# Performance work log

Measured on AMD Instinct MI355X. Metric: run time of the kernel, lower is better.

Reference implementation:

```python
import jax, jax.numpy as jnp
import numpy as np

B, S, H, E = 64, 1024, 256, 256

def setup_inputs() -> dict:
    key = jax.random.key(0)
    k = jax.random.split(key, 6)
    scale = 1.0 / np.sqrt(H)
    return {
        "data_alpha": jax.random.normal(k[0], (B, S, H), jnp.float32),
        "data_beta": jax.random.normal(k[1], (B, S, H), jnp.float32),
        "data_embed": jax.random.normal(k[2], (B, S, E), jnp.float32),
        "data_mask": jnp.ones((B, S), jnp.float32),
        "Wb": jax.random.normal(k[3], (E, H), jnp.float32) * scale,
        "bb": jnp.zeros((E,), jnp.float32),
        "Wa": jax.random.normal(k[4], (H,), jnp.float32) * scale,
        "ba": jnp.zeros((1,), jnp.float32),
    }

def reference(data_alpha, data_beta, data_embed, data_mask, Wb, bb, Wa, ba):
    # beta gates: tanh(Linear(H->E))  [B,S,E]
    beta_w = jnp.tanh(jnp.einsum('bsh,eh->bse', data_beta, Wb) + bb)
    # alpha logits: Linear(H->1)  [B,S]
    corr = jnp.einsum('bsh,h->bs', data_alpha, Wa) + ba
    attn = jnp.exp(corr)[:, None, :]                       # [B,1,S]
    seq = data_alpha.shape[1]
    flag = jnp.triu(jnp.ones((seq, seq), data_alpha.dtype))[None]  # j >= i
    ef = flag * data_mask[:, None, :]                      # [B,S,S]
    num = attn * ef                                        # [B,S,S]
    acc = jnp.sum(num, axis=-1, keepdims=True) + 1e-10     # [B,S,1]
    alpha = num / acc                                      # [B,S,S]
    ew = beta_w * data_embed                               # [B,S,E]
    return jnp.einsum('bij,bje->bie', alpha, ew)           # [B,S,E]
```

## Files before the change

### kernel.cpp

```cpp
#include <hip/hip_runtime.h>
#include <hip/hip_bf16.h>

#define S_LEN 1024
#define B_DIM 64
#define H_DIM 256
#define E_DIM 256
#define M_ROWS (B_DIM * S_LEN)

#define CT_COLS 64
#define NCT (E_DIM / CT_COLS)
#define CHUNK_R 256
#define NCHUNKS (S_LEN / CHUNK_R)
#define NTHREADS 1024
#define NWAVES 16

#define BPAD 264

typedef __attribute__((ext_vector_type(8))) short bf16x8;
typedef __attribute__((ext_vector_type(4))) float f32x4;

__device__ __forceinline__ short cvt1(float f) {
  union { float ff; unsigned u; } t;
  t.ff = f;
  unsigned u = t.u;
  return (short)((u + 0x7fffu + ((u >> 16) & 1u)) >> 16);
}

__device__ __forceinline__ bf16x8 cvt8v(float4 x, float4 y) {
  bf16x8 r;
  r[0] = cvt1(x.x); r[1] = cvt1(x.y); r[2] = cvt1(x.z); r[3] = cvt1(x.w);
  r[4] = cvt1(y.x); r[5] = cvt1(y.y); r[6] = cvt1(y.z); r[7] = cvt1(y.w);
  return r;
}

__device__ __forceinline__ float fast_tanh(float x) {
  float t = __expf(2.0f * x);
  return 1.0f - 2.0f * __builtin_amdgcn_rcpf(t + 1.0f);
}

__global__ __launch_bounds__(256) void w_kernel(
    const float* __restrict__ alpha, const float* __restrict__ Wa,
    const float* __restrict__ ba, const float* __restrict__ mask,
    float* __restrict__ wv) {
  int wave = threadIdx.x >> 6, lane = threadIdx.x & 63;
  long long row = (long long)blockIdx.x * 4 + wave;
  const float4 a = reinterpret_cast<const float4*>(alpha + row * H_DIM)[lane];
  const float4 wa = reinterpret_cast<const float4*>(Wa)[lane];
  float d = a.x * wa.x + a.y * wa.y + a.z * wa.z + a.w * wa.w;
#pragma unroll
  for (int m = 32; m; m >>= 1) d += __shfl_xor(d, m);
  if (lane == 0) wv[row] = expf(d + ba[0]) * mask[row];
}

__global__ __launch_bounds__(1024) void acc_kernel(
    const float* __restrict__ wv, float* __restrict__ invacc) {
  __shared__ float s[2][S_LEN];
  int b = blockIdx.x, i = threadIdx.x;
  s[0][i] = wv[b * S_LEN + i];
  __syncthreads();
  int src = 0;
#pragma unroll
  for (int off = 1; off < S_LEN; off <<= 1) {
    float v = s[src][i];
    if (i + off < S_LEN) v += s[src][i + off];
    s[src ^ 1][i] = v;
    __syncthreads();
    src ^= 1;
  }
  invacc[b * S_LEN + i] = 1.0f / (s[src][i] + 1e-10f);
}

__global__ __launch_bounds__(NTHREADS, 8) void fused_kernel(
    const float* __restrict__ beta, const float* __restrict__ Wb,
    const float* __restrict__ bb, const float* __restrict__ embed,
    const float* __restrict__ wv, const float* __restrict__ invacc,
    float* __restrict__ out) {
  __shared__ short Bsm[CT_COLS * BPAD];
  __shared__ float segsum[NWAVES * CT_COLS];
  __shared__ float carry[CT_COLS];

  const int tid = threadIdx.x;
  const int hw = blockIdx.x;
  const int b = (hw & 7) + (((hw >> 3) & 7) << 3);
  const int colbase = (hw >> 6) * CT_COLS;

  {
    int c = tid >> 4, ks = (tid & 15) * 16;
    const float4* src =
        reinterpret_cast<const float4*>(Wb + (long long)(colbase + c) * H_DIM + ks);
    float4 v0 = src[0], v1 = src[1], v2 = src[2], v3 = src[3];
    *reinterpret_cast<bf16x8*>(&Bsm[c * BPAD + ks]) = cvt8v(v0, v1);
    *reinterpret_cast<bf16x8*>(&Bsm[c * BPAD + ks + 8]) = cvt8v(v2, v3);
  }
  if (tid < CT_COLS) carry[tid] = 0.f;
  __syncthreads();

  const int wave = tid >> 6, lane = tid & 63;
  const int rl = lane & 15, kg = lane >> 4;

  for (int chunk = NCHUNKS - 1; chunk >= 0; --chunk) {
    const long long rowstart = (long long)b * S_LEN + chunk * CHUNK_R;
    const long long r0 = rowstart + wave * 16;
    const float* aptr = beta + (r0 + rl) * H_DIM + kg * 8;

    f32x4 acc[4] = {{0.f,0.f,0.f,0.f},{0.f,0.f,0.f,0.f},
                    {0.f,0.f,0.f,0.f},{0.f,0.f,0.f,0.f}};

    float4 a0[2], a1[2];
    a0[0] = *reinterpret_cast<const float4*>(aptr + 0);
    a1[0] = *reinterpret_cast<const float4*>(aptr + 4);
    a0[1] = *reinterpret_cast<const float4*>(aptr + 32);
    a1[1] = *reinterpret_cast<const float4*>(aptr + 36);
#pragma unroll
    for (int ks = 0; ks < 8; ++ks) {
      float4 na0 = {0.f,0.f,0.f,0.f}, na1 = {0.f,0.f,0.f,0.f};
      if (ks < 6) {
        na0 = *reinterpret_cast<const float4*>(aptr + (ks + 2) * 32);
        na1 = *reinterpret_cast<const float4*>(aptr + (ks + 2) * 32 + 4);
      }
      bf16x8 am = cvt8v(a0[0], a1[0]);
      int kb = ks * 32 + kg * 8;
#pragma unroll
      for (int j = 0; j < 4; ++j) {
        bf16x8 bn = *reinterpret_cast<const bf16x8*>(&Bsm[(j * 16 + rl) * BPAD + kb]);
        acc[j] = __builtin_amdgcn_mfma_f32_16x16x32_bf16(am, bn, acc[j], 0, 0, 0);
      }
      a0[0] = a0[1]; a1[0] = a1[1];
      a0[1] = na0;   a1[1] = na1;
    }

    float wvq[4], inv[4];
#pragma unroll
    for (int q = 0; q < 4; ++q) {
      long long r = r0 + kg * 4 + q;
      wvq[q] = wv[r];
      inv[q] = invacc[r];
    }

    float sv[4][4];
    float off[4];
    float cn[4];
#pragma unroll
    for (int j = 0; j < 4; ++j) {
      int c = j * 16 + rl;
      int e = colbase + c;
      float bbe = bb[e];
      float p[4];
#pragma unroll
      for (int q = 0; q < 4; ++q) {
        long long r = r0 + kg * 4 + q;
        p[q] = wvq[q] * fast_tanh(acc[j][q] + bbe) * embed[r * E_DIM + e];
      }
      sv[j][3] = p[3];
      sv[j][2] = p[2] + sv[j][3];
      sv[j][1] = p[1] + sv[j][2];
      sv[j][0] = p[0] + sv[j][1];
      float gtot = sv[j][0];
      float t16 = __shfl_xor(gtot, 16);
      float t32 = __shfl_xor(gtot, 32);
      float t48 = __shfl_xor(gtot, 48);
      off[j] = (kg == 0) ? (t16 + t32 + t48)
             : (kg == 1) ? (t32 + t48)
             : (kg == 2) ? t16 : 0.f;
      float wtot = gtot + t16 + t32 + t48;
      if (kg == 0) segsum[wave * CT_COLS + c] = wtot;
    }
    __syncthreads();

#pragma unroll
    for (int j = 0; j < 4; ++j) {
      int c = j * 16 + rl;
      float segoff = carry[c];
      for (int w2 = wave + 1; w2 < NWAVES; ++w2)
        segoff += segsum[w2 * CT_COLS + c];
      off[j] += segoff;
      cn[j] = off[j] + sv[j][0];
#pragma unroll
      for (int q = 0; q < 4; ++q) {
        long long r = r0 + kg * 4 + q;
        out[r * E_DIM + colbase + c] = (sv[j][q] + off[j]) * inv[q];
      }
    }
    __syncthreads();
    if (wave == 0 && kg == 0) {
#pragma unroll
      for (int j = 0; j < 4; ++j) carry[j * 16 + rl] = cn[j];
    }
  }
}

extern "C" void kernel_launch(void* const* d_in, const int* in_sizes, int n_in,
                              void* d_out, int out_size, void* d_ws,
                              size_t ws_size, hipStream_t stream) {
  const float* alpha = (const float*)d_in[0];
  const float* beta = (const float*)d_in[1];
  const float* embed = (const float*)d_in[2];
  const float* mask = (const float*)d_in[3];
  const float* Wb = (const float*)d_in[4];
  const float* bb = (const float*)d_in[5];
  const float* Wa = (const float*)d_in[6];
  const float* ba = (const float*)d_in[7];
  float* out = (float*)d_out;

  float* wv = (float*)d_ws;
  float* invacc = wv + M_ROWS;

  w_kernel<<<M_ROWS / 4, 256, 0, stream>>>(alpha, Wa, ba, mask, wv);
  acc_kernel<<<B_DIM, 1024, 0, stream>>>(wv, invacc);
  fused_kernel<<<B_DIM * NCT, NTHREADS, 0, stream>>>(beta, Wb, bb, embed, wv,
                                                     invacc, out);
}
```

Baseline: 259.5 us.

## Prefetch next chunk's beta, embed and weights; double-buffer scan scratch to drop a barrier

Loads of the next chunk's beta rows, embed values, wv and invacc are issued during the current chunk's compute, so global-memory latency overlaps the MFMA and scan work. The segment-sum and carry arrays are double-buffered by chunk parity, which removes the second __syncthreads per chunk. The bias loads are hoisted out of the loop, the cross-wave offset loop is fully unrolled with a predicate, and the occupancy hint in launch bounds drops from 8 to 4. The extra prefetch registers raise register pressure, and the lower occupancy hint changes how many waves the compiler plans for.

Result: faster. 242.9 us (-6.4%).

```diff
diff --git a/kernel.cpp b/kernel.cpp
--- a/kernel.cpp
+++ b/kernel.cpp
@@ -70,14 +70,14 @@
   invacc[b * S_LEN + i] = 1.0f / (s[src][i] + 1e-10f);
 }
 
-__global__ __launch_bounds__(NTHREADS, 8) void fused_kernel(
+__global__ __launch_bounds__(NTHREADS, 4) void fused_kernel(
     const float* __restrict__ beta, const float* __restrict__ Wb,
     const float* __restrict__ bb, const float* __restrict__ embed,
     const float* __restrict__ wv, const float* __restrict__ invacc,
     float* __restrict__ out) {
   __shared__ short Bsm[CT_COLS * BPAD];
-  __shared__ float segsum[NWAVES * CT_COLS];
-  __shared__ float carry[CT_COLS];
+  __shared__ float segsum[2][NWAVES * CT_COLS];
+  __shared__ float carry[2][CT_COLS];
 
   const int tid = threadIdx.x;
   const int hw = blockIdx.x;
@@ -92,65 +92,89 @@
     *reinterpret_cast<bf16x8*>(&Bsm[c * BPAD + ks]) = cvt8v(v0, v1);
     *reinterpret_cast<bf16x8*>(&Bsm[c * BPAD + ks + 8]) = cvt8v(v2, v3);
   }
-  if (tid < CT_COLS) carry[tid] = 0.f;
+  if (tid < CT_COLS) { carry[0][tid] = 0.f; carry[1][tid] = 0.f; }
   __syncthreads();
 
   const int wave = tid >> 6, lane = tid & 63;
   const int rl = lane & 15, kg = lane >> 4;
 
+  float bbv[4];
+#pragma unroll
+  for (int j = 0; j < 4; ++j) bbv[j] = bb[colbase + j * 16 + rl];
+
+  const float* ap =
+      beta + ((long long)b * S_LEN + 3 * CHUNK_R + wave * 16 + rl) * H_DIM + kg * 8;
+  float4 pa0 = *reinterpret_cast<const float4*>(ap + 0);
+  float4 pa1 = *reinterpret_cast<const float4*>(ap + 4);
+  float4 pb0 = *reinterpret_cast<const float4*>(ap + 32);
+  float4 pb1 = *reinterpret_cast<const float4*>(ap + 36);
+
+  float emb[4][4], wvq[4], inv[4];
+  {
+    const long long r0 = (long long)b * S_LEN + 3 * CHUNK_R + wave * 16 + kg * 4;
+#pragma unroll
+    for (int q = 0; q < 4; ++q) {
+      wvq[q] = wv[r0 + q];
+      inv[q] = invacc[r0 + q];
+#pragma unroll
+      for (int j = 0; j < 4; ++j)
+        emb[q][j] = embed[(r0 + q) * E_DIM + colbase + j * 16 + rl];
+    }
+  }
+
   for (int chunk = NCHUNKS - 1; chunk >= 0; --chunk) {
+    const int nc = (chunk > 0) ? chunk - 1 : 0;
     const long long rowstart = (long long)b * S_LEN + chunk * CHUNK_R;
     const long long r0 = rowstart + wave * 16;
-    const float* aptr = beta + (r0 + rl) * H_DIM + kg * 8;
+    const float* ap_next =
+        beta + ((long long)b * S_LEN + nc * CHUNK_R + wave * 16 + rl) * H_DIM + kg * 8;
 
     f32x4 acc[4] = {{0.f,0.f,0.f,0.f},{0.f,0.f,0.f,0.f},
                     {0.f,0.f,0.f,0.f},{0.f,0.f,0.f,0.f}};
 
-    float4 a0[2], a1[2];
-    a0[0] = *reinterpret_cast<const float4*>(aptr + 0);
-    a1[0] = *reinterpret_cast<const float4*>(aptr + 4);
-    a0[1] = *reinterpret_cast<const float4*>(aptr + 32);
-    a1[1] = *reinterpret_cast<const float4*>(aptr + 36);
 #pragma unroll
     for (int ks = 0; ks < 8; ++ks) {
-      float4 na0 = {0.f,0.f,0.f,0.f}, na1 = {0.f,0.f,0.f,0.f};
+      float4 n0, n1;
       if (ks < 6) {
-        na0 = *reinterpret_cast<const float4*>(aptr + (ks + 2) * 32);
-        na1 = *reinterpret_cast<const float4*>(aptr + (ks + 2) * 32 + 4);
-      }
-      bf16x8 am = cvt8v(a0[0], a1[0]);
+        n0 = *reinterpret_cast<const float4*>(ap + (ks + 2) * 32);
+        n1 = *reinterpret_cast<const float4*>(ap + (ks + 2) * 32 + 4);
+      } else {
+        n0 = *reinterpret_cast<const float4*>(ap_next + (ks - 6) * 32);
+        n1 = *reinterpret_cast<const float4*>(ap_next + (ks - 6) * 32 + 4);
+      }
+      bf16x8 am = cvt8v(pa0, pa1);
       int kb = ks * 32 + kg * 8;
 #pragma unroll
       for (int j = 0; j < 4; ++j) {
         bf16x8 bn = *reinterpret_cast<const bf16x8*>(&Bsm[(j * 16 + rl) * BPAD + kb]);
         acc[j] = __builtin_amdgcn_mfma_f32_16x16x32_bf16(am, bn, acc[j], 0, 0, 0);
       }
-      a0[0] = a0[1]; a1[0] = a1[1];
-      a0[1] = na0;   a1[1] = na1;
-    }
-
-    float wvq[4], inv[4];
-#pragma unroll
-    for (int q = 0; q < 4; ++q) {
-      long long r = r0 + kg * 4 + q;
-      wvq[q] = wv[r];
-      inv[q] = invacc[r];
-    }
-
-    float sv[4][4];
-    float off[4];
-    float cn[4];
+      pa0 = pb0; pa1 = pb1; pb0 = n0; pb1 = n1;
+    }
+    ap = ap_next;
+
+    float emb_n[4][4], wvq_n[4], inv_n[4];
+    {
+      const long long rn = (long long)b * S_LEN + nc * CHUNK_R + wave * 16 + kg * 4;
+#pragma unroll
+      for (int q = 0; q < 4; ++q) {
+        wvq_n[q] = wv[rn + q];
+        inv_n[q] = invacc[rn + q];
+#pragma unroll
+        for (int j = 0; j < 4; ++j)
+          emb_n[q][j] = embed[(rn + q) * E_DIM + colbase + j * 16 + rl];
+      }
+    }
+
+    const int rd = chunk & 1;
+    float sv[4][4], off[4];
 #pragma unroll
     for (int j = 0; j < 4; ++j) {
       int c = j * 16 + rl;
-      int e = colbase + c;
-      float bbe = bb[e];
       float p[4];
 #pragma unroll
-      for (int q = 0; q < 4; ++q) {
-        long long r = r0 + kg * 4 + q;
-        p[q] = wvq[q] * fast_tanh(acc[j][q] + bbe) * embed[r * E_DIM + e];
-      }
+      for (int q = 0; q < 4; ++q)
+        p[q] = wvq[q] * fast_tanh(acc[j][q] + bbv[j]) * emb[q][j];
       sv[j][3] = p[3];
       sv[j][2] = p[2] + sv[j][3];
       sv[j][1] = p[1] + sv[j][2];
@@ -163,28 +187,33 @@
              : (kg == 1) ? (t32 + t48)
              : (kg == 2) ? t16 : 0.f;
       float wtot = gtot + t16 + t32 + t48;
-      if (kg == 0) segsum[wave * CT_COLS + c] = wtot;
+      if (kg == 0) segsum[rd][wave * CT_COLS + c] = wtot;
     }
     __syncthreads();
 
 #pragma unroll
     for (int j = 0; j < 4; ++j) {
       int c = j * 16 + rl;
-      float segoff = carry[c];
-      for (int w2 = wave + 1; w2 < NWAVES; ++w2)
-        segoff += segsum[w2 * CT_COLS + c];
+      float segoff = carry[rd][c];
+#pragma unroll
+      for (int w2 = 0; w2 < NWAVES; ++w2) {
+        float t = segsum[rd][w2 * CT_COLS + c];
+        segoff += (w2 > wave) ? t : 0.f;
+      }
       off[j] += segoff;
-      cn[j] = off[j] + sv[j][0];
+      if (wave == 0 && kg == 0) carry[rd ^ 1][c] = off[j] + sv[j][0];
 #pragma unroll
       for (int q = 0; q < 4; ++q) {
         long long r = r0 + kg * 4 + q;
         out[r * E_DIM + colbase + c] = (sv[j][q] + off[j]) * inv[q];
       }
     }
-    __syncthreads();
-    if (wave == 0 && kg == 0) {
-#pragma unroll
-      for (int j = 0; j < 4; ++j) carry[j * 16 + rl] = cn[j];
+
+#pragma unroll
+    for (int q = 0; q < 4; ++q) {
+      wvq[q] = wvq_n[q]; inv[q] = inv_n[q];
+#pragma unroll
+      for (int j = 0; j < 4; ++j) emb[q][j] = emb_n[q][j];
     }
   }
 }
```
